# Kernel tuning notes

Hardware: AMD Instinct MI355X
Metric: run time of the kernel (lower is better)

The kernel has to match this reference:

```python
import jax, jax.numpy as jnp
import numpy as np

D_MODEL = 1024
N_HEADS = 16
HEAD_DIM = D_MODEL // N_HEADS


def setup_inputs() -> dict:
    key = jax.random.key(0)
    ks = jax.random.split(key, 5)
    B, T = 2, 2048
    x = jax.random.normal(ks[0], (B, T, D_MODEL), dtype=jnp.float32)
    s_in = 1.0 / np.sqrt(D_MODEL)
    W_qkv = jax.random.normal(ks[1], (D_MODEL, 3 * D_MODEL), dtype=jnp.float32) * s_in
    b_qkv = jnp.zeros((3 * D_MODEL,), dtype=jnp.float32)
    W_out = jax.random.normal(ks[2], (D_MODEL, D_MODEL), dtype=jnp.float32) * s_in
    b_out = jnp.zeros((D_MODEL,), dtype=jnp.float32)
    return {"x": x, "W_qkv": W_qkv, "b_qkv": b_qkv, "W_out": W_out, "b_out": b_out}


def reference(x, W_qkv, b_qkv, W_out, b_out):
    B, T, C = x.shape
    qkv = x @ W_qkv + b_qkv  # (B, T, 3C)
    q, k, v = jnp.split(qkv, 3, axis=-1)
    # (B, H, T, Dh)
    q = q.reshape(B, T, N_HEADS, HEAD_DIM).transpose(0, 2, 1, 3)
    k = k.reshape(B, T, N_HEADS, HEAD_DIM).transpose(0, 2, 1, 3)
    v = v.reshape(B, T, N_HEADS, HEAD_DIM).transpose(0, 2, 1, 3)
    scale = 1.0 / jnp.sqrt(jnp.asarray(HEAD_DIM, dtype=x.dtype))
    scores = jnp.einsum('bhqd,bhkd->bhqk', q, k) * scale  # (B, H, T, T)
    causal = jnp.tril(jnp.ones((T, T), dtype=bool))
    scores = jnp.where(causal[None, None], scores, jnp.asarray(-jnp.inf, dtype=scores.dtype))
    attn = jax.nn.softmax(scores, axis=-1)
    out = jnp.einsum('bhqk,bhkd->bhqd', attn, v)  # (B, H, T, Dh)
    out = out.transpose(0, 2, 1, 3).reshape(B, T, C)
    return out @ W_out + b_out
```

## Files before the change

### kernel.cpp

```cpp
#include <hip/hip_runtime.h>
#include <hip/hip_bf16.h>
#include <stdint.h>

typedef __bf16 bf16;
typedef __bf16 bf16x4 __attribute__((ext_vector_type(4)));
typedef __bf16 bf16x8 __attribute__((ext_vector_type(8)));
typedef float  f32x4  __attribute__((ext_vector_type(4)));

#define D_MODEL 1024
#define N_HEADS 16
#define HEAD_DIM 64
#define SEQ 2048
#define BATCH 2
#define LOG2E 1.4426950408889634f
#define NEG_SENT -3.0e4f
#define CAP 24.0f

__device__ __forceinline__ bf16x8 ld8(const bf16* p) { return *(const bf16x8*)p; }

__device__ __forceinline__ void async16(const bf16* g, bf16* l) {
  __builtin_amdgcn_global_load_lds(
      (const __attribute__((address_space(1))) void*)g,
      (__attribute__((address_space(3))) void*)l, 16, 0, 0);
}

__global__ __launch_bounds__(256)
void prep(const float* __restrict__ x, bf16* __restrict__ x16,
          const float* __restrict__ Wqkv, bf16* __restrict__ Wqkv_t,
          const float* __restrict__ Wout, bf16* __restrict__ Wout_t) {
  __shared__ float tile[32][33];
  const int blk = blockIdx.x, tid = threadIdx.x;
  if (blk < 4096) {
    int i = (blk * 256 + tid) * 4;
    float4 v = *(const float4*)&x[i];
    bf16 o[4] = {(bf16)v.x, (bf16)v.y, (bf16)v.z, (bf16)v.w};
    *(uint2*)&x16[i] = *(uint2*)o;
    return;
  }
  const float* in; bf16* out; int R, C, c0, r0;
  if (blk < 7168) {
    int b = blk - 4096;
    in = Wqkv; out = Wqkv_t; R = 1024; C = 3072;
    c0 = (b % 96) * 32; r0 = (b / 96) * 32;
  } else {
    int b = blk - 7168;
    in = Wout; out = Wout_t; R = 1024; C = 1024;
    c0 = (b % 32) * 32; r0 = (b / 32) * 32;
  }
  const int tx = tid & 31, ty = tid >> 5;
  #pragma unroll
  for (int i = 0; i < 32; i += 8)
    tile[ty + i][tx] = in[(size_t)(r0 + ty + i) * C + c0 + tx];
  __syncthreads();
  #pragma unroll
  for (int i = 0; i < 32; i += 8)
    out[(size_t)(c0 + ty + i) * R + r0 + tx] = (bf16)tile[tx][ty + i];
}

__global__ __launch_bounds__(256)
void gemm_bt(const bf16* __restrict__ A, const bf16* __restrict__ Bt,
             const float* __restrict__ bias, float* __restrict__ outf,
             bf16* __restrict__ Qp, bf16* __restrict__ Kp, bf16* __restrict__ Vtp,
             int N, int mode) {
  __shared__ __align__(16) bf16 shA[128 * 32];
  __shared__ __align__(16) bf16 shB[128 * 32];
  const int tid  = threadIdx.x;
  const int bm0  = blockIdx.y * 128, bn0 = blockIdx.x * 128;
  const int wave = tid >> 6, lane = tid & 63;
  const int quad = lane >> 4, l16 = lane & 15;
  const int wm = (wave >> 1) * 64, wn = (wave & 1) * 64;

  const int c_lo  = tid;
  const int row_lo = c_lo >> 2,  col_lo = (c_lo & 3) << 3;
  const int c_hi  = tid + 256;
  const int row_hi = c_hi >> 2,  col_hi = (c_hi & 3) << 3;
  const int cb_lo = (wave * 64) * 8;
  const int cb_hi = (256 + wave * 64) * 8;

  f32x4 acc[4][4];
  #pragma unroll
  for (int i = 0; i < 4; i++)
    #pragma unroll
    for (int j = 0; j < 4; j++)
      acc[i][j] = (f32x4){0.f, 0.f, 0.f, 0.f};

  for (int k0 = 0; k0 < 1024; k0 += 32) {
    async16(&A[(size_t)(bm0 + row_lo) * 1024 + k0 + col_lo], &shA[cb_lo]);
    async16(&A[(size_t)(bm0 + row_hi) * 1024 + k0 + col_hi], &shA[cb_hi]);
    async16(&Bt[(size_t)(bn0 + row_lo) * 1024 + k0 + col_lo], &shB[cb_lo]);
    async16(&Bt[(size_t)(bn0 + row_hi) * 1024 + k0 + col_hi], &shB[cb_hi]);
    __syncthreads();
    bf16x8 af[4], bg[4];
    #pragma unroll
    for (int i = 0; i < 4; i++)
      af[i] = ld8(&shA[(wm + i * 16 + l16) * 32 + quad * 8]);
    #pragma unroll
    for (int j = 0; j < 4; j++)
      bg[j] = ld8(&shB[(wn + j * 16 + l16) * 32 + quad * 8]);
    #pragma unroll
    for (int i = 0; i < 4; i++)
      #pragma unroll
      for (int j = 0; j < 4; j++)
        acc[i][j] = __builtin_amdgcn_mfma_f32_16x16x32_bf16(af[i], bg[j], acc[i][j], 0, 0, 0);
    __syncthreads();
  }

  #pragma unroll
  for (int i = 0; i < 4; i++) {
    #pragma unroll
    for (int j = 0; j < 4; j++) {
      int gn = bn0 + wn + j * 16 + l16;
      float bv = bias[gn];
      int gm0 = bm0 + wm + i * 16 + quad * 4;
      if (mode == 1) {
        #pragma unroll
        for (int r = 0; r < 4; r++)
          outf[(size_t)(gm0 + r) * N + gn] = acc[i][j][r] + bv;
      } else {
        int which = gn >> 10, rem = gn & 1023;
        int h = rem >> 6, d = rem & 63;
        int b = gm0 >> 11, t0 = gm0 & 2047;
        int bh = b * N_HEADS + h;
        if (which == 2) {
          bf16x4 vv = {(bf16)(acc[i][j][0] + bv), (bf16)(acc[i][j][1] + bv),
                       (bf16)(acc[i][j][2] + bv), (bf16)(acc[i][j][3] + bv)};
          *(bf16x4*)&Vtp[((size_t)bh * 64 + d) * SEQ + t0] = vv;
        } else {
          bf16* dst = (which == 0) ? Qp : Kp;
          #pragma unroll
          for (int r = 0; r < 4; r++)
            dst[((size_t)bh * SEQ + t0 + r) * 64 + d] = (bf16)(acc[i][j][r] + bv);
        }
      }
    }
  }
}

__global__ __launch_bounds__(256)
void attn_k(const bf16* __restrict__ Qp, const bf16* __restrict__ Kp,
            const bf16* __restrict__ Vtp, bf16* __restrict__ Obuf) {
  __shared__ __align__(16) bf16 shK[2][64 * 64];
  __shared__ __align__(16) bf16 shV[2][64 * 64];
  __shared__ __align__(16) bf16 shPT[4][32 * 72];
  const int tid  = threadIdx.x;
  const int wave = tid >> 6, lane = tid & 63;
  const int quad = lane >> 4, l16 = lane & 15;
  const int bx = blockIdx.x;
  const int qb = 15 - (bx >> 5);
  const int bh = bx & 31;
  const int qw0 = qb * 128 + wave * 32;

  const bf16* Qbh = Qp  + (size_t)bh * SEQ * 64;
  const bf16* Kbh = Kp  + (size_t)bh * SEQ * 64;
  const bf16* Vbh = Vtp + (size_t)bh * 64 * SEQ;

  const int kr_s = tid >> 3, kc_s = tid & 7;

  bf16x8 aQ[2][2];
  #pragma unroll
  for (int g = 0; g < 2; g++)
    #pragma unroll
    for (int p = 0; p < 2; p++)
      aQ[g][p] = ld8(&Qbh[(size_t)(qw0 + g * 16 + l16) * 64 + p * 32 + quad * 8]);

  f32x4 o0[4], o1[4];
  #pragma unroll
  for (int j = 0; j < 4; j++) { o0[j] = (f32x4){0.f,0.f,0.f,0.f}; o1[j] = (f32x4){0.f,0.f,0.f,0.f}; }
  f32x4 lacc0 = (f32x4){0.f,0.f,0.f,0.f}, lacc1 = (f32x4){0.f,0.f,0.f,0.f};
  const int qlane0 = qw0 + l16, qlane1 = qw0 + 16 + l16;
  const int xq = l16 & 7;

  const float SC = 0.125f * LOG2E;
  bf16* PT = shPT[wave];

  #pragma unroll
  for (int i = 0; i < 2; i++) {
    int kr = kr_s + i * 32;
    async16(&Kbh[(size_t)kr * 64 + (kc_s ^ (kr & 7)) * 8], &shK[0][(kr * 8 + kc_s) * 8]);
    async16(&Vbh[(size_t)kr * SEQ + (kc_s ^ (kr & 7)) * 8], &shV[0][(kr * 8 + kc_s) * 8]);
  }
  __syncthreads();

  const int NS = 2 * qb + 2;
  int cur = 0;
  for (int s = 0; s < NS; s++) {
    if (s + 1 < NS) {
      const int kb1 = (s + 1) * 64;
      #pragma unroll
      for (int i = 0; i < 2; i++) {
        int kr = kr_s + i * 32;
        async16(&Kbh[(size_t)(kb1 + kr) * 64 + (kc_s ^ (kr & 7)) * 8],
                &shK[cur ^ 1][(kr * 8 + kc_s) * 8]);
        async16(&Vbh[(size_t)kr * SEQ + kb1 + (kc_s ^ (kr & 7)) * 8],
                &shV[cur ^ 1][(kr * 8 + kc_s) * 8]);
      }
    }

    const int hb = s * 64;
    if (hb <= qw0 + 31) {
      const bf16* Kb = shK[cur];
      const bf16* Vb = shV[cur];

      f32x4 st0[4], st1[4];
      __builtin_amdgcn_s_setprio(1);
      #pragma unroll
      for (int c = 0; c < 4; c++) {
        int kr0 = c * 16 + l16;
        bf16x8 kf0 = ld8(&Kb[kr0 * 64 + ((quad    ) ^ xq) * 8]);
        bf16x8 kf1 = ld8(&Kb[kr0 * 64 + ((quad + 4) ^ xq) * 8]);
        f32x4 a0 = (f32x4){0.f,0.f,0.f,0.f};
        a0 = __builtin_amdgcn_mfma_f32_16x16x32_bf16(kf0, aQ[0][0], a0, 0, 0, 0);
        a0 = __builtin_amdgcn_mfma_f32_16x16x32_bf16(kf1, aQ[0][1], a0, 0, 0, 0);
        f32x4 a1 = (f32x4){0.f,0.f,0.f,0.f};
        a1 = __builtin_amdgcn_mfma_f32_16x16x32_bf16(kf0, aQ[1][0], a1, 0, 0, 0);
        a1 = __builtin_amdgcn_mfma_f32_16x16x32_bf16(kf1, aQ[1][1], a1, 0, 0, 0);
        st0[c] = a0; st1[c] = a1;
      }
      __builtin_amdgcn_s_setprio(0);

      if (hb + 63 > qw0) {
        #pragma unroll
        for (int c = 0; c < 4; c++)
          #pragma unroll
          for (int r = 0; r < 4; r++) {
            int key = hb + c * 16 + quad * 4 + r;
            if (key > qlane0) st0[c][r] = NEG_SENT;
            if (key > qlane1) st1[c][r] = NEG_SENT;
          }
      }

      #pragma unroll
      for (int c = 0; c < 4; c++) {
        #pragma unroll
        for (int r = 0; r < 4; r++) {
          st0[c][r] = exp2f(__builtin_fmaf(st0[c][r], SC, -CAP));
          st1[c][r] = exp2f(__builtin_fmaf(st1[c][r], SC, -CAP));
        }
        lacc0 += st0[c]; lacc1 += st1[c];
      }

      #pragma unroll
      for (int c = 0; c < 4; c++) {
        bf16x4 p0 = {(bf16)st0[c][0], (bf16)st0[c][1], (bf16)st0[c][2], (bf16)st0[c][3]};
        bf16x4 p1 = {(bf16)st1[c][0], (bf16)st1[c][1], (bf16)st1[c][2], (bf16)st1[c][3]};
        *(bf16x4*)&PT[l16 * 72 + c * 16 + quad * 4] = p0;
        *(bf16x4*)&PT[(16 + l16) * 72 + c * 16 + quad * 4] = p1;
      }
      asm volatile("s_waitcnt lgkmcnt(0)" ::: "memory");
      bf16x8 bP00 = ld8(&PT[l16 * 72 + quad * 8]);
      bf16x8 bP01 = ld8(&PT[l16 * 72 + 32 + quad * 8]);
      bf16x8 bP10 = ld8(&PT[(16 + l16) * 72 + quad * 8]);
      bf16x8 bP11 = ld8(&PT[(16 + l16) * 72 + 32 + quad * 8]);

      __builtin_amdgcn_s_setprio(1);
      #pragma unroll
      for (int j = 0; j < 4; j++) {
        int d = j * 16 + l16;
        bf16x8 v0 = ld8(&Vb[d * 64 + ((quad    ) ^ xq) * 8]);
        bf16x8 v1 = ld8(&Vb[d * 64 + ((quad + 4) ^ xq) * 8]);
        o0[j] = __builtin_amdgcn_mfma_f32_16x16x32_bf16(v0, bP00, o0[j], 0, 0, 0);
        o0[j] = __builtin_amdgcn_mfma_f32_16x16x32_bf16(v1, bP01, o0[j], 0, 0, 0);
        o1[j] = __builtin_amdgcn_mfma_f32_16x16x32_bf16(v0, bP10, o1[j], 0, 0, 0);
        o1[j] = __builtin_amdgcn_mfma_f32_16x16x32_bf16(v1, bP11, o1[j], 0, 0, 0);
      }
      __builtin_amdgcn_s_setprio(0);
    }

    __syncthreads();
    cur ^= 1;
  }

  const int b = bh >> 4, h = bh & 15;
  {
    float lr0 = (lacc0[0] + lacc0[1]) + (lacc0[2] + lacc0[3]);
    lr0 += __shfl_xor(lr0, 16, 64);
    lr0 += __shfl_xor(lr0, 32, 64);
    float lr1 = (lacc1[0] + lacc1[1]) + (lacc1[2] + lacc1[3]);
    lr1 += __shfl_xor(lr1, 16, 64);
    lr1 += __shfl_xor(lr1, 32, 64);
    float inv0 = 1.0f / lr0, inv1 = 1.0f / lr1;
    size_t base0 = ((size_t)(b * SEQ + qw0 + l16)) * D_MODEL + h * 64;
    size_t base1 = ((size_t)(b * SEQ + qw0 + 16 + l16)) * D_MODEL + h * 64;
    #pragma unroll
    for (int j = 0; j < 4; j++) {
      bf16x4 ov0 = {(bf16)(o0[j][0] * inv0), (bf16)(o0[j][1] * inv0),
                    (bf16)(o0[j][2] * inv0), (bf16)(o0[j][3] * inv0)};
      bf16x4 ov1 = {(bf16)(o1[j][0] * inv1), (bf16)(o1[j][1] * inv1),
                    (bf16)(o1[j][2] * inv1), (bf16)(o1[j][3] * inv1)};
      *(bf16x4*)&Obuf[base0 + j * 16 + quad * 4] = ov0;
      *(bf16x4*)&Obuf[base1 + j * 16 + quad * 4] = ov1;
    }
  }
}

extern "C" void kernel_launch(void* const* d_in, const int* in_sizes, int n_in,
                              void* d_out, int out_size, void* d_ws, size_t ws_size,
                              hipStream_t stream) {
  const float* x    = (const float*)d_in[0];
  const float* Wqkv = (const float*)d_in[1];
  const float* bqkv = (const float*)d_in[2];
  const float* Wout = (const float*)d_in[3];
  const float* bout = (const float*)d_in[4];
  float* out = (float*)d_out;

  char* ws = (char*)d_ws;
  bf16* x16    = (bf16*)(ws);
  bf16* Wqkv_t = (bf16*)(ws + 8388608);
  bf16* Wout_t = (bf16*)(ws + 14680064);
  bf16* Qp     = (bf16*)(ws + 16777216);
  bf16* Kp     = (bf16*)(ws + 25165824);
  bf16* Vtp    = (bf16*)(ws + 33554432);
  bf16* Obuf   = x16;

  prep<<<8192, 256, 0, stream>>>(x, x16, Wqkv, Wqkv_t, Wout, Wout_t);

  gemm_bt<<<dim3(3072 / 128, 4096 / 128), 256, 0, stream>>>(
      x16, Wqkv_t, bqkv, nullptr, Qp, Kp, Vtp, 3072, 0);

  attn_k<<<dim3(512), 256, 0, stream>>>(Qp, Kp, Vtp, Obuf);

  gemm_bt<<<dim3(1024 / 128, 4096 / 128), 256, 0, stream>>>(
      Obuf, Wout_t, bout, out, nullptr, nullptr, nullptr, 1024, 1);
}
```

Measured before the change: 201.6 us.

## Double GEMM K-step to 64 and stage epilogue through LDS for coalesced stores

The GEMM now loads 64-wide K slices per barrier pair instead of 32, which halves the number of syncthreads and global_load_lds rounds. The epilogue for the output projection and for the Q/K head-major layout now stages results in a shared-memory arena and writes full rows as 16-byte vector stores rather than scattered scalar stores. The V-transpose path is unchanged apart from hoisting the per-block index computation. In exchange, shared memory grows to 34 KB per block, which may lower occupancy, and the epilogue adds extra barriers.

```diff
diff --git a/kernel.cpp b/kernel.cpp
--- a/kernel.cpp
+++ b/kernel.cpp
@@ -62,21 +62,15 @@
              const float* __restrict__ bias, float* __restrict__ outf,
              bf16* __restrict__ Qp, bf16* __restrict__ Kp, bf16* __restrict__ Vtp,
              int N, int mode) {
-  __shared__ __align__(16) bf16 shA[128 * 32];
-  __shared__ __align__(16) bf16 shB[128 * 32];
+  __shared__ __align__(16) char arena[34816];
+  bf16* shA = (bf16*)arena;
+  bf16* shB = (bf16*)(arena + 16384);
   const int tid  = threadIdx.x;
   const int bm0  = blockIdx.y * 128, bn0 = blockIdx.x * 128;
   const int wave = tid >> 6, lane = tid & 63;
   const int quad = lane >> 4, l16 = lane & 15;
   const int wm = (wave >> 1) * 64, wn = (wave & 1) * 64;
 
-  const int c_lo  = tid;
-  const int row_lo = c_lo >> 2,  col_lo = (c_lo & 3) << 3;
-  const int c_hi  = tid + 256;
-  const int row_hi = c_hi >> 2,  col_hi = (c_hi & 3) << 3;
-  const int cb_lo = (wave * 64) * 8;
-  const int cb_hi = (256 + wave * 64) * 8;
-
   f32x4 acc[4][4];
   #pragma unroll
   for (int i = 0; i < 4; i++)
@@ -84,54 +78,106 @@
     for (int j = 0; j < 4; j++)
       acc[i][j] = (f32x4){0.f, 0.f, 0.f, 0.f};
 
-  for (int k0 = 0; k0 < 1024; k0 += 32) {
-    async16(&A[(size_t)(bm0 + row_lo) * 1024 + k0 + col_lo], &shA[cb_lo]);
-    async16(&A[(size_t)(bm0 + row_hi) * 1024 + k0 + col_hi], &shA[cb_hi]);
-    async16(&Bt[(size_t)(bn0 + row_lo) * 1024 + k0 + col_lo], &shB[cb_lo]);
-    async16(&Bt[(size_t)(bn0 + row_hi) * 1024 + k0 + col_hi], &shB[cb_hi]);
+  const int sr = lane >> 3, sc = (lane & 7) * 8;
+  for (int k0 = 0; k0 < 1024; k0 += 64) {
+    #pragma unroll
+    for (int is = 0; is < 4; is++) {
+      int r0 = (is * 4 + wave) * 8;
+      async16(&A[(size_t)(bm0 + r0 + sr) * 1024 + k0 + sc], &shA[r0 * 64]);
+      async16(&Bt[(size_t)(bn0 + r0 + sr) * 1024 + k0 + sc], &shB[r0 * 64]);
+    }
     __syncthreads();
-    bf16x8 af[4], bg[4];
-    #pragma unroll
-    for (int i = 0; i < 4; i++)
-      af[i] = ld8(&shA[(wm + i * 16 + l16) * 32 + quad * 8]);
-    #pragma unroll
-    for (int j = 0; j < 4; j++)
-      bg[j] = ld8(&shB[(wn + j * 16 + l16) * 32 + quad * 8]);
-    #pragma unroll
-    for (int i = 0; i < 4; i++)
+    #pragma unroll
+    for (int kk = 0; kk < 2; kk++) {
+      bf16x8 af[4], bg[4];
+      #pragma unroll
+      for (int i = 0; i < 4; i++)
+        af[i] = ld8(&shA[(wm + i * 16 + l16) * 64 + kk * 32 + quad * 8]);
       #pragma unroll
       for (int j = 0; j < 4; j++)
-        acc[i][j] = __builtin_amdgcn_mfma_f32_16x16x32_bf16(af[i], bg[j], acc[i][j], 0, 0, 0);
+        bg[j] = ld8(&shB[(wn + j * 16 + l16) * 64 + kk * 32 + quad * 8]);
+      #pragma unroll
+      for (int i = 0; i < 4; i++)
+        #pragma unroll
+        for (int j = 0; j < 4; j++)
+          acc[i][j] = __builtin_amdgcn_mfma_f32_16x16x32_bf16(af[i], bg[j], acc[i][j], 0, 0, 0);
+    }
     __syncthreads();
   }
 
-  #pragma unroll
-  for (int i = 0; i < 4; i++) {
-    #pragma unroll
-    for (int j = 0; j < 4; j++) {
-      int gn = bn0 + wn + j * 16 + l16;
-      float bv = bias[gn];
-      int gm0 = bm0 + wm + i * 16 + quad * 4;
-      if (mode == 1) {
-        #pragma unroll
-        for (int r = 0; r < 4; r++)
-          outf[(size_t)(gm0 + r) * N + gn] = acc[i][j][r] + bv;
-      } else {
-        int which = gn >> 10, rem = gn & 1023;
+  const int which = bn0 >> 10;
+  const int b = bm0 >> 11, t0 = bm0 & 2047;
+
+  if (mode == 0 && which == 2) {
+    #pragma unroll
+    for (int i = 0; i < 4; i++) {
+      #pragma unroll
+      for (int j = 0; j < 4; j++) {
+        int gn = bn0 + wn + j * 16 + l16;
+        float bv = bias[gn];
+        int rem = gn & 1023;
         int h = rem >> 6, d = rem & 63;
-        int b = gm0 >> 11, t0 = gm0 & 2047;
+        int gm0 = bm0 + wm + i * 16 + quad * 4;
+        int tt = gm0 & 2047;
         int bh = b * N_HEADS + h;
-        if (which == 2) {
-          bf16x4 vv = {(bf16)(acc[i][j][0] + bv), (bf16)(acc[i][j][1] + bv),
-                       (bf16)(acc[i][j][2] + bv), (bf16)(acc[i][j][3] + bv)};
-          *(bf16x4*)&Vtp[((size_t)bh * 64 + d) * SEQ + t0] = vv;
-        } else {
-          bf16* dst = (which == 0) ? Qp : Kp;
+        bf16x4 vv = {(bf16)(acc[i][j][0] + bv), (bf16)(acc[i][j][1] + bv),
+                     (bf16)(acc[i][j][2] + bv), (bf16)(acc[i][j][3] + bv)};
+        *(bf16x4*)&Vtp[((size_t)bh * 64 + d) * SEQ + tt] = vv;
+      }
+    }
+  } else if (mode == 1) {
+    float* Cf = (float*)arena;
+    #pragma unroll
+    for (int h = 0; h < 2; h++) {
+      if ((wave & 1) == h) {
+        #pragma unroll
+        for (int i = 0; i < 4; i++)
           #pragma unroll
-          for (int r = 0; r < 4; r++)
-            dst[((size_t)bh * SEQ + t0 + r) * 64 + d] = (bf16)(acc[i][j][r] + bv);
-        }
-      }
+          for (int j = 0; j < 4; j++) {
+            float bv = bias[bn0 + h * 64 + j * 16 + l16];
+            #pragma unroll
+            for (int r = 0; r < 4; r++)
+              Cf[(wm + i * 16 + quad * 4 + r) * 68 + j * 16 + l16] = acc[i][j][r] + bv;
+          }
+      }
+      __syncthreads();
+      #pragma unroll
+      for (int k = 0; k < 8; k++) {
+        int u = k * 256 + tid;
+        int row = u >> 4, ch = u & 15;
+        float4 v = *(const float4*)&Cf[row * 68 + ch * 4];
+        *(float4*)&outf[(size_t)(bm0 + row) * N + bn0 + h * 64 + ch * 4] = v;
+      }
+      __syncthreads();
+    }
+  } else {
+    bf16* Cb = (bf16*)arena;
+    const int hbase = (bn0 & 1023) >> 6;
+    #pragma unroll
+    for (int h = 0; h < 2; h++) {
+      if ((wave & 1) == h) {
+        #pragma unroll
+        for (int i = 0; i < 4; i++)
+          #pragma unroll
+          for (int j = 0; j < 4; j++) {
+            float bv = bias[bn0 + h * 64 + j * 16 + l16];
+            #pragma unroll
+            for (int r = 0; r < 4; r++)
+              Cb[(wm + i * 16 + quad * 4 + r) * 72 + j * 16 + l16] =
+                  (bf16)(acc[i][j][r] + bv);
+          }
+      }
+      __syncthreads();
+      bf16* dst = (which == 0) ? Qp : Kp;
+      const size_t base = ((size_t)(b * N_HEADS + hbase + h) * SEQ + t0) * 64;
+      #pragma unroll
+      for (int k = 0; k < 4; k++) {
+        int u = k * 256 + tid;
+        int row = u >> 3, ch = u & 7;
+        bf16x8 v = ld8(&Cb[row * 72 + ch * 8]);
+        *(bf16x8*)&dst[base + (size_t)row * 64 + ch * 8] = v;
+      }
+      __syncthreads();
     }
   }
 }
```

Result: slower. 222.7 us (+10.5%).
